# Kernel tuning notes

Measured on AMD Instinct MI355X. Metric: run time of the kernel, lower is better.

Reference implementation:

```python
import jax, jax.numpy as jnp
import numpy as np

N_NODES = 100000
N_EDGES = 3200000
D_FEAT = 128
N1 = 128
N2 = 64
NUM_CLASSES = 10
NUM_GRAPHS = 256


def gcn_conv(x, edge_index, W, b, num_nodes):
    """PyG GCNConv: y = D^-1/2 (A+I) D^-1/2 (x W) + b, self-loops added."""
    src, dst = edge_index[0], edge_index[1]
    # degree including self-loop (edge weight 1)
    deg = jax.ops.segment_sum(jnp.ones_like(dst, dtype=x.dtype), dst,
                              num_segments=num_nodes) + 1.0
    dis = jnp.where(deg > 0, deg ** -0.5, 0.0)  # deg_inv_sqrt, [N]
    h = x @ W                                    # transform first, [N, out]
    norm = dis[src] * dis[dst]                   # [E]
    msg = h[src] * norm[:, None]                 # gather + scale, [E, out]
    agg = jax.ops.segment_sum(msg, dst, num_segments=num_nodes)
    agg = agg + h * (dis * dis)[:, None]         # self-loop contribution
    return agg + b


def global_mean_pool(x, batch, num_graphs):
    sums = jax.ops.segment_sum(x, batch, num_segments=num_graphs)
    cnt = jax.ops.segment_sum(jnp.ones((x.shape[0],), dtype=x.dtype), batch,
                              num_segments=num_graphs)
    return sums / jnp.maximum(cnt, 1.0)[:, None]


def setup_inputs() -> dict:
    key = jax.random.key(0)
    ks = jax.random.split(key, 8)
    x = jax.random.normal(ks[0], (N_NODES, D_FEAT), dtype=jnp.float32)
    edge_index = jax.random.randint(ks[1], (2, N_EDGES), 0, N_NODES, dtype=jnp.int64)
    batch = jnp.sort(jax.random.randint(ks[2], (N_NODES,), 0, NUM_GRAPHS, dtype=jnp.int64))
    W1 = jax.random.normal(ks[3], (D_FEAT, N1), dtype=jnp.float32) / np.sqrt(D_FEAT)
    b1 = jnp.zeros((N1,), dtype=jnp.float32)
    W2 = jax.random.normal(ks[4], (N1, N2), dtype=jnp.float32) / np.sqrt(N1)
    b2 = jnp.zeros((N2,), dtype=jnp.float32)
    Wfc = jax.random.normal(ks[5], (N2, NUM_CLASSES), dtype=jnp.float32) / np.sqrt(N2)
    bfc = jnp.zeros((NUM_CLASSES,), dtype=jnp.float32)
    return {"x": x, "edge_index": edge_index, "batch": batch,
            "W1": W1, "b1": b1, "W2": W2, "b2": b2,
            "Wfc": Wfc, "bfc": bfc, "num_graphs": NUM_GRAPHS}


def reference(x, edge_index, batch, W1, b1, W2, b2, Wfc, bfc, num_graphs):
    n = x.shape[0]
    h = gcn_conv(x, edge_index, W1, b1, n)
    h = jax.nn.relu(h)
    h = gcn_conv(h, edge_index, W2, b2, n)
    g = global_mean_pool(h, batch, num_graphs)   # [num_graphs, N2]
    # dropout is identity at inference
    return g @ Wfc + bfc                          # [num_graphs, num_classes]
```

## Files before the change

kernel.cpp:

```cpp
#include <hip/hip_runtime.h>
#include <math.h>

typedef unsigned int  u32;
typedef unsigned short u16;

#define TILE1 8192
#define BKW   256
#define CAP   9216

typedef __attribute__((ext_vector_type(8))) short bf16x8;
typedef __attribute__((ext_vector_type(4))) float f32x4;
union frag_u { bf16x8 v; u32 u[4]; uint4 q; };

__device__ inline u32 bf16_rne(float f) {
    u32 u = __float_as_uint(f);
    return (u + 0x7FFFu + ((u >> 16) & 1u)) >> 16;
}
__device__ inline float bf_lo(u32 u) { return __uint_as_float(u << 16); }
__device__ inline float bf_hi(u32 u) { return __uint_as_float(u & 0xFFFF0000u); }

__device__ inline void add8(float* acc, uint4 q) {
    acc[0] += bf_lo(q.x); acc[1] += bf_hi(q.x);
    acc[2] += bf_lo(q.y); acc[3] += bf_hi(q.y);
    acc[4] += bf_lo(q.z); acc[5] += bf_hi(q.z);
    acc[6] += bf_lo(q.w); acc[7] += bf_hi(q.w);
}

__device__ inline u32 relu_pk(u32 v) {
    u32 s = v & 0x80008000u;
    u32 m = (s >> 15) * 0xFFFFu;
    return v & ~m;
}


__global__ __launch_bounds__(512) void k_part1(const int* __restrict__ ei,
                                               int* __restrict__ bucketCur,
                                               u32* __restrict__ tmp,
                                               int E, int N, int NBK) {
    __shared__ int hist[1024];
    __shared__ int base[512];
    const int tid = threadIdx.x;
    if (tid < NBK) { hist[tid] = 0; hist[512 + tid] = 0; }
    __syncthreads();

    const int rep = (tid & 1) << 9;
    const int t0 = blockIdx.x * TILE1;
    const int4* ei4s = (const int4*)ei;
    const int4* ei4d = (const int4*)(ei + E);
    const int q0 = t0 >> 2;
    const int QE = E >> 2;

    int sv[16], dv[16], key[16];
#pragma unroll
    for (int j = 0; j < 4; ++j) {
        int qi = q0 + j * 512 + tid;
        int4 s4 = make_int4(0, 0, 0, 0), d4 = make_int4(-1, -1, -1, -1);
        if (qi < QE) { s4 = ei4s[qi]; d4 = ei4d[qi]; }
        sv[4 * j + 0] = s4.x; dv[4 * j + 0] = d4.x;
        sv[4 * j + 1] = s4.y; dv[4 * j + 1] = d4.y;
        sv[4 * j + 2] = s4.z; dv[4 * j + 2] = d4.z;
        sv[4 * j + 3] = s4.w; dv[4 * j + 3] = d4.w;
    }
#pragma unroll
    for (int j = 0; j < 16; ++j) {
        key[j] = -1;
        if ((unsigned)dv[j] < (unsigned)N && (unsigned)sv[j] < (unsigned)N) {
            key[j] = dv[j] >> 8;
            atomicAdd(&hist[key[j] + rep], 1);
        }
    }
    __syncthreads();
    if (tid < NBK) {
        int tot = hist[tid] + hist[512 + tid];
        base[tid] = atomicAdd(&bucketCur[tid], tot);
        hist[tid] = 0;
    }
    __syncthreads();
#pragma unroll
    for (int j = 0; j < 16; ++j) {
        if (key[j] >= 0) {
            int slot = atomicAdd(&hist[key[j]], 1);
            int off = base[key[j]] + slot;
            if (off < CAP)
                tmp[(size_t)key[j] * CAP + off] =
                    ((u32)(dv[j] & 255) << 17) | (u32)sv[j];
        }
    }
}

__global__ __launch_bounds__(512) void k_part2(const int* __restrict__ bucketCnt,
                                               const u32* __restrict__ tmp,
                                               int* __restrict__ csr,
                                               int* __restrict__ rowptr,
                                               float* __restrict__ dis,
                                               int N, int NBK) {
    __shared__ int hist[256];
    __shared__ int ts[512];
    __shared__ int sStart;
    const int b = blockIdx.x;
    const int t = threadIdx.x;

    int myCnt = (t < NBK) ? bucketCnt[t] : 0;
    ts[t] = myCnt;
    __syncthreads();
    for (int off = 1; off < 512; off <<= 1) {
        int u = (t >= off) ? ts[t - off] : 0;
        __syncthreads();
        ts[t] += u;
        __syncthreads();
    }
    if (t == b) sStart = ts[t] - myCnt;
    if (b == 0 && t == NBK - 1) rowptr[N] = ts[t];
    __syncthreads();
    const int start = sStart;
    const int cnt = bucketCnt[b];
    const u32* src = tmp + (size_t)b * CAP;

    if (t < 256) hist[t] = 0;
    __syncthreads();
    for (int i = t; i < cnt; i += 512)
        atomicAdd(&hist[src[i] >> 17], 1);
    __syncthreads();

    int h = (t < 256) ? hist[t] : 0;
    ts[t] = h;
    __syncthreads();
    for (int off = 1; off < 512; off <<= 1) {
        int u = (t >= off) ? ts[t - off] : 0;
        __syncthreads();
        ts[t] += u;
        __syncthreads();
    }
    if (t < 256) hist[t] = ts[t] - h;
    __syncthreads();

    if (t < 256) {
        int gn = (b << 8) + t;
        if (gn < N) {
            int e0 = hist[t];
            int e1 = (t < 255) ? hist[t + 1] : cnt;
            rowptr[gn] = start + e0;
            dis[gn] = rsqrtf((float)(e1 - e0) + 1.0f);
        }
    }
    __syncthreads();

    for (int i = t; i < cnt; i += 512) {
        u32 v = src[i];
        int p = atomicAdd(&hist[v >> 17], 1);
        csr[start + p] = (int)(v & 0x1FFFFu);
    }
}


__global__ __launch_bounds__(256) void k_convW(
    const float* __restrict__ W1, const float* __restrict__ W2,
    u32* __restrict__ W1h, u32* __restrict__ W1l,
    u32* __restrict__ W2h, u32* __restrict__ W2l,
    int* __restrict__ bucketCur, int NBK)
{
    int idx = blockIdx.x * 256 + threadIdx.x;
    if (idx < NBK) bucketCur[idx] = 0;
    if (idx < 8192) {
        int n = idx >> 6, k = (idx & 63) * 2;
        float w0 = W1[k * 128 + n], w1 = W1[(k + 1) * 128 + n];
        u32 h0 = bf16_rne(w0), h1 = bf16_rne(w1);
        u32 l0 = bf16_rne(w0 - __uint_as_float(h0 << 16));
        u32 l1 = bf16_rne(w1 - __uint_as_float(h1 << 16));
        W1h[idx] = h0 | (h1 << 16);
        W1l[idx] = l0 | (l1 << 16);
    } else if (idx < 12288) {
        int i2 = idx - 8192;
        int n = i2 >> 6, k = (i2 & 63) * 2;
        float w0 = W2[k * 64 + n], w1 = W2[(k + 1) * 64 + n];
        u32 h0 = bf16_rne(w0), h1 = bf16_rne(w1);
        u32 l0 = bf16_rne(w0 - __uint_as_float(h0 << 16));
        u32 l1 = bf16_rne(w1 - __uint_as_float(h1 << 16));
        W2h[i2] = h0 | (h1 << 16);
        W2l[i2] = l0 | (l1 << 16);
    }
}


__global__ __launch_bounds__(256) void k_gemm1m(
    const float* __restrict__ X, const u32* __restrict__ Wh,
    const u32* __restrict__ Wl, const float* __restrict__ dis,
    u32* __restrict__ Hb, int M)
{
    __shared__ uint4 sW[2176];
    const int tid = threadIdx.x;
    const int ny = blockIdx.y;
    const uint4* Wh4 = (const uint4*)Wh;
    const uint4* Wl4 = (const uint4*)Wl;
#pragma unroll
    for (int i = 0; i < 4; ++i) {
        int idx = tid + i * 256;
        int l = idx >> 4, j = idx & 15;
        sW[l * 17 + j] = Wh4[(ny * 64 + l) * 16 + j];
        sW[1088 + l * 17 + j] = Wl4[(ny * 64 + l) * 16 + j];
    }
    __syncthreads();

    const int w = tid >> 6, lane = tid & 63;
    const int mrow = blockIdx.x * 64 + w * 16;
    const int m16 = lane & 15, quad = lane >> 4;
    int gm = mrow + m16; if (gm >= M) gm = M - 1;

    frag_u Ah[4], Al[4];
    const float* xr = X + (size_t)gm * 128;
#pragma unroll
    for (int kt = 0; kt < 4; ++kt) {
        int kb = kt * 32 + quad * 8;
        float4 xa = *(const float4*)(xr + kb);
        float4 xb = *(const float4*)(xr + kb + 4);
        float xe[8] = {xa.x, xa.y, xa.z, xa.w, xb.x, xb.y, xb.z, xb.w};
#pragma unroll
        for (int j = 0; j < 4; ++j) {
            u32 h0 = bf16_rne(xe[2 * j]),     h1 = bf16_rne(xe[2 * j + 1]);
            u32 l0 = bf16_rne(xe[2 * j]     - __uint_as_float(h0 << 16));
            u32 l1 = bf16_rne(xe[2 * j + 1] - __uint_as_float(h1 << 16));
            Ah[kt].u[j] = h0 | (h1 << 16);
            Al[kt].u[j] = l0 | (l1 << 16);
        }
    }

    float dv[4];
#pragma unroll
    for (int r = 0; r < 4; ++r) {
        int gR = mrow + quad * 4 + r;
        dv[r] = (gR < M) ? dis[gR] : 0.f;
    }

#pragma unroll
    for (int nt = 0; nt < 4; ++nt) {
        f32x4 acc = {0.f, 0.f, 0.f, 0.f};
        int l = nt * 16 + m16;
#pragma unroll
        for (int kt = 0; kt < 4; ++kt) {
            frag_u Bh, Bl;
            Bh.q = sW[l * 17 + kt * 4 + quad];
            Bl.q = sW[1088 + l * 17 + kt * 4 + quad];
            acc = __builtin_amdgcn_mfma_f32_16x16x32_bf16(Al[kt].v, Bh.v, acc, 0, 0, 0);
            acc = __builtin_amdgcn_mfma_f32_16x16x32_bf16(Ah[kt].v, Bl.v, acc, 0, 0, 0);
            acc = __builtin_amdgcn_mfma_f32_16x16x32_bf16(Ah[kt].v, Bh.v, acc, 0, 0, 0);
        }
#pragma unroll
        for (int r = 0; r < 4; ++r) {
            float vs = acc[r] * dv[r];
            float vo = __shfl_xor(vs, 1, 64);
            if ((m16 & 1) == 0) {
                int gR = mrow + quad * 4 + r;
                if (gR < M)
                    Hb[(size_t)gR * 64 + ny * 32 + nt * 8 + (m16 >> 1)] =
                        bf16_rne(vs) | (bf16_rne(vo) << 16);
            }
        }
    }
}


__global__ __launch_bounds__(256) void k_gemm2m(
    const u32* __restrict__ Xb, const u32* __restrict__ Wh,
    const u32* __restrict__ Wl, const float* __restrict__ dis,
    u32* __restrict__ Hb, int M)
{
    __shared__ uint4 sW[2176];
    const int tid = threadIdx.x;
    const uint4* Wh4 = (const uint4*)Wh;
    const uint4* Wl4 = (const uint4*)Wl;
#pragma unroll
    for (int i = 0; i < 4; ++i) {
        int idx = tid + i * 256;
        int l = idx >> 4, j = idx & 15;
        sW[l * 17 + j] = Wh4[l * 16 + j];
        sW[1088 + l * 17 + j] = Wl4[l * 16 + j];
    }
    __syncthreads();

    const int w = tid >> 6, lane = tid & 63;
    const int mrow = blockIdx.x * 64 + w * 16;
    const int m16 = lane & 15, quad = lane >> 4;
    int gm = mrow + m16; if (gm >= M) gm = M - 1;

    const uint4* X4 = (const uint4*)Xb;
    frag_u A[4];
#pragma unroll
    for (int kt = 0; kt < 4; ++kt) {
        A[kt].q = X4[(size_t)gm * 16 + kt * 4 + quad];
#pragma unroll
        for (int j = 0; j < 4; ++j) A[kt].u[j] = relu_pk(A[kt].u[j]);
    }

    float dv[4];
#pragma unroll
    for (int r = 0; r < 4; ++r) {
        int gR = mrow + quad * 4 + r;
        dv[r] = (gR < M) ? dis[gR] : 0.f;
    }

#pragma unroll
    for (int nt = 0; nt < 4; ++nt) {
        f32x4 acc = {0.f, 0.f, 0.f, 0.f};
        int l = nt * 16 + m16;
#pragma unroll
        for (int kt = 0; kt < 4; ++kt) {
            frag_u Bh, Bl;
            Bh.q = sW[l * 17 + kt * 4 + quad];
            Bl.q = sW[1088 + l * 17 + kt * 4 + quad];
            acc = __builtin_amdgcn_mfma_f32_16x16x32_bf16(A[kt].v, Bl.v, acc, 0, 0, 0);
            acc = __builtin_amdgcn_mfma_f32_16x16x32_bf16(A[kt].v, Bh.v, acc, 0, 0, 0);
        }
#pragma unroll
        for (int r = 0; r < 4; ++r) {
            float vs = acc[r] * dv[r];
            float vo = __shfl_xor(vs, 1, 64);
            if ((m16 & 1) == 0) {
                int gR = mrow + quad * 4 + r;
                if (gR < M)
                    Hb[(size_t)gR * 32 + nt * 8 + (m16 >> 1)] =
                        bf16_rne(vs) | (bf16_rne(vo) << 16);
            }
        }
    }
}


template <int PART>
__global__ __launch_bounds__(256) void k_agg1h(
    const int* __restrict__ rowptr, const int* __restrict__ csr,
    const float* __restrict__ dis, const uint4* __restrict__ Hb4,
    const float* __restrict__ bias, u32* __restrict__ AGGb, int N)
{
    int n = (blockIdx.x * 256 + threadIdx.x) >> 6;
    int lane = threadIdx.x & 63;
    int slot = lane >> 3;
    int li   = lane & 7;
    if (n >= N) return;
    int e = rowptr[n];
    const int s1 = rowptr[n + 1];
    const float dn = dis[n];
    const int q = PART * 8 + li;

    float acc[8];
#pragma unroll
    for (int j = 0; j < 8; ++j) acc[j] = 0.f;

    for (; e + 16 <= s1; e += 16) {
        int i0 = csr[e + slot];
        int i1 = csr[e + 8 + slot];
        uint4 q0 = Hb4[(size_t)i0 * 16 + q];
        uint4 q1 = Hb4[(size_t)i1 * 16 + q];
        add8(acc, q0); add8(acc, q1);
    }
    for (; e + 8 <= s1; e += 8) {
        int i0 = csr[e + slot];
        uint4 q0 = Hb4[(size_t)i0 * 16 + q];
        add8(acc, q0);
    }
    {
        int rem = s1 - e;
        int idx = -1;
        if (slot < rem) idx = csr[e + slot];
        else if (slot == rem) idx = n;
        if (idx >= 0) {
            uint4 qq = Hb4[(size_t)idx * 16 + q];
            add8(acc, qq);
        }
    }

#pragma unroll
    for (int j = 0; j < 8; ++j) {
        acc[j] += __shfl_xor(acc[j], 8, 64);
        acc[j] += __shfl_xor(acc[j], 16, 64);
        acc[j] += __shfl_xor(acc[j], 32, 64);
    }

    if (slot < 2) {
        float4 bv = ((const float4*)bias)[q * 2 + slot];
        float o0 = fmaf(dn, acc[4 * slot + 0], bv.x);
        float o1 = fmaf(dn, acc[4 * slot + 1], bv.y);
        float o2 = fmaf(dn, acc[4 * slot + 2], bv.z);
        float o3 = fmaf(dn, acc[4 * slot + 3], bv.w);
        uint2 p;
        p.x = bf16_rne(o0) | (bf16_rne(o1) << 16);
        p.y = bf16_rne(o2) | (bf16_rne(o3) << 16);
        ((uint2*)AGGb)[(size_t)n * 32 + q * 2 + slot] = p;
    }
}


__global__ __launch_bounds__(256) void k_agg2(
    const int* __restrict__ rowptr, const int* __restrict__ csr,
    const float* __restrict__ dis, const uint4* __restrict__ Hb4,
    const float* __restrict__ bias, u32* __restrict__ AGGb, int N)
{
    int n = (blockIdx.x * 256 + threadIdx.x) >> 6;
    int lane = threadIdx.x & 63;
    int slot = lane >> 3;
    int li   = lane & 7;
    if (n >= N) return;
    int e = rowptr[n];
    const int s1 = rowptr[n + 1];
    const float dn = dis[n];

    float acc[8];
#pragma unroll
    for (int j = 0; j < 8; ++j) acc[j] = 0.f;

    for (; e + 16 <= s1; e += 16) {
        int i0 = csr[e + slot];
        int i1 = csr[e + 8 + slot];
        uint4 q0 = Hb4[(size_t)i0 * 8 + li];
        uint4 q1 = Hb4[(size_t)i1 * 8 + li];
        add8(acc, q0); add8(acc, q1);
    }
    for (; e + 8 <= s1; e += 8) {
        int i0 = csr[e + slot];
        uint4 q0 = Hb4[(size_t)i0 * 8 + li];
        add8(acc, q0);
    }
    {
        int rem = s1 - e;
        int idx = -1;
        if (slot < rem) idx = csr[e + slot];
        else if (slot == rem) idx = n;
        if (idx >= 0) {
            uint4 q = Hb4[(size_t)idx * 8 + li];
            add8(acc, q);
        }
    }

#pragma unroll
    for (int j = 0; j < 8; ++j) {
        acc[j] += __shfl_xor(acc[j], 8, 64);
        acc[j] += __shfl_xor(acc[j], 16, 64);
        acc[j] += __shfl_xor(acc[j], 32, 64);
    }

    if (slot < 2) {
        float4 bv = ((const float4*)bias)[li * 2 + slot];
        float o0 = fmaf(dn, acc[4 * slot + 0], bv.x);
        float o1 = fmaf(dn, acc[4 * slot + 1], bv.y);
        float o2 = fmaf(dn, acc[4 * slot + 2], bv.z);
        float o3 = fmaf(dn, acc[4 * slot + 3], bv.w);
        uint2 p;
        p.x = bf16_rne(o0) | (bf16_rne(o1) << 16);
        p.y = bf16_rne(o2) | (bf16_rne(o3) << 16);
        ((uint2*)AGGb)[(size_t)n * 16 + li * 2 + slot] = p;
    }
}


__device__ inline int lower_bound(const int* __restrict__ b, int n, int v) {
    int lo = 0, hi = n;
    while (lo < hi) { int m = (lo + hi) >> 1; if (b[m] < v) lo = m + 1; else hi = m; }
    return lo;
}

__global__ __launch_bounds__(256) void k_poolfc(
    const int* __restrict__ batch, const u32* __restrict__ AGGb2,
    const float* __restrict__ Wfc, const float* __restrict__ bfc,
    float* __restrict__ out, int n)
{
    int g = blockIdx.x;
    int start = lower_bound(batch, n, g);
    int end   = lower_bound(batch, n, g + 1);
    int tid = threadIdx.x;
    int f = tid & 63, stripe = tid >> 6;
    int ui = f >> 1, hi = f & 1;
    float acc = 0.f;
    for (int i = start + stripe; i < end; i += 4) {
        u32 v = AGGb2[(size_t)i * 32 + ui];
        acc += hi ? bf_hi(v) : bf_lo(v);
    }
    __shared__ float red[256];
    __shared__ float mean[64];
    red[tid] = acc;
    __syncthreads();
    if (tid < 64) {
        float s = red[tid] + red[tid + 64] + red[tid + 128] + red[tid + 192];
        float c = (float)(end - start);
        mean[tid] = s / fmaxf(c, 1.0f);
    }
    __syncthreads();
    if (tid < 10) {
        float o = bfc[tid];
        for (int k = 0; k < 64; ++k)
            o = fmaf(mean[k], Wfc[k * 10 + tid], o);
        out[g * 10 + tid] = o;
    }
}


extern "C" void kernel_launch(void* const* d_in, const int* in_sizes, int n_in,
                              void* d_out, int out_size, void* d_ws, size_t ws_size,
                              hipStream_t stream)
{
    const float* x    = (const float*)d_in[0];
    const int*   ei   = (const int*)d_in[1];
    const int*   batch= (const int*)d_in[2];
    const float* W1   = (const float*)d_in[3];
    const float* b1   = (const float*)d_in[4];
    const float* W2   = (const float*)d_in[5];
    const float* b2   = (const float*)d_in[6];
    const float* Wfc  = (const float*)d_in[7];
    const float* bfc  = (const float*)d_in[8];
    float* out = (float*)d_out;

    const int N  = in_sizes[0] / 128;
    const int E  = in_sizes[1] / 2;
    const int ng = out_size / 10;

    const int NBK = (N + BKW - 1) / BKW;

    int*   rowptr    = (int*)d_ws;
    int*   bucketCur = rowptr + 102400;
    float* dis       = (float*)(bucketCur + 512);
    int*   csr       = (int*)(dis + 102400);
    u32*   tmp       = (u32*)(csr + E);
    u32*   Hb1       = tmp;
    u32*   agg2b     = tmp;
    u32*   agg1b     = (u32*)((int*)tmp + (size_t)N * 64);
    u16*   Hb2       = (u16*)((int*)agg1b + (size_t)N * 128);
    u32*   W1h       = (u32*)((int*)Hb2 + (size_t)N * 32);
    u32*   W1l       = W1h + 8192;
    u32*   W2h       = W1l + 8192;
    u32*   W2l       = W2h + 4096;

    k_convW<<<48, 256, 0, stream>>>(W1, W2, W1h, W1l, W2h, W2l, bucketCur, NBK);
    k_part1<<<(E + TILE1 - 1) / TILE1, 512, 0, stream>>>(ei, bucketCur, tmp, E, N, NBK);
    k_part2<<<NBK, 512, 0, stream>>>(bucketCur, tmp, csr, rowptr, dis, N, NBK);

    k_gemm1m<<<dim3((N + 63) / 64, 2), 256, 0, stream>>>(x, W1h, W1l, dis, Hb1, N);
    k_agg1h<0><<<(N + 3) / 4, 256, 0, stream>>>(rowptr, csr, dis, (const uint4*)Hb1, b1, agg1b, N);
    k_agg1h<1><<<(N + 3) / 4, 256, 0, stream>>>(rowptr, csr, dis, (const uint4*)Hb1, b1, agg1b, N);

    k_gemm2m<<<(N + 63) / 64, 256, 0, stream>>>(agg1b, W2h, W2l, dis, (u32*)Hb2, N);
    k_agg2<<<(N + 3) / 4, 256, 0, stream>>>(rowptr, csr, dis, (const uint4*)Hb2, b2, agg2b, N);

    k_poolfc<<<ng, 256, 0, stream>>>(batch, agg2b, Wfc, bfc, out, N);
}
```

Before: 398.8 us.

## Fuse weight bf16 split into GEMMs, merge agg1 halves, widen partition histogram

```diff
diff --git a/kernel.cpp b/kernel.cpp
--- a/kernel.cpp
+++ b/kernel.cpp
@@ -32,18 +32,26 @@
     return v & ~m;
 }
 
+__device__ inline void split_pk(float w0, float w1, u32& hp, u32& lp) {
+    u32 h0 = bf16_rne(w0), h1 = bf16_rne(w1);
+    u32 l0 = bf16_rne(w0 - __uint_as_float(h0 << 16));
+    u32 l1 = bf16_rne(w1 - __uint_as_float(h1 << 16));
+    hp = h0 | (h1 << 16);
+    lp = l0 | (l1 << 16);
+}
+
 
 __global__ __launch_bounds__(512) void k_part1(const int* __restrict__ ei,
                                                int* __restrict__ bucketCur,
                                                u32* __restrict__ tmp,
                                                int E, int N, int NBK) {
-    __shared__ int hist[1024];
-    __shared__ int base[512];
+    __shared__ int cnt[2048];
+    __shared__ int base[2048];
     const int tid = threadIdx.x;
-    if (tid < NBK) { hist[tid] = 0; hist[512 + tid] = 0; }
-    __syncthreads();
-
-    const int rep = (tid & 1) << 9;
+    for (int i = tid; i < 2048; i += 512) cnt[i] = 0;
+    __syncthreads();
+
+    const int rep = tid & 3;
     const int t0 = blockIdx.x * TILE1;
     const int4* ei4s = (const int4*)ei;
     const int4* ei4d = (const int4*)(ei + E);
@@ -66,21 +74,28 @@
         key[j] = -1;
         if ((unsigned)dv[j] < (unsigned)N && (unsigned)sv[j] < (unsigned)N) {
             key[j] = dv[j] >> 8;
-            atomicAdd(&hist[key[j] + rep], 1);
+            atomicAdd(&cnt[key[j] * 4 + rep], 1);
         }
     }
     __syncthreads();
     if (tid < NBK) {
-        int tot = hist[tid] + hist[512 + tid];
-        base[tid] = atomicAdd(&bucketCur[tid], tot);
-        hist[tid] = 0;
+        int c0 = cnt[tid * 4], c1 = cnt[tid * 4 + 1];
+        int c2 = cnt[tid * 4 + 2], c3 = cnt[tid * 4 + 3];
+        int b0 = atomicAdd(&bucketCur[tid], c0 + c1 + c2 + c3);
+        base[tid * 4 + 0] = b0;
+        base[tid * 4 + 1] = b0 + c0;
+        base[tid * 4 + 2] = b0 + c0 + c1;
+        base[tid * 4 + 3] = b0 + c0 + c1 + c2;
+        cnt[tid * 4 + 0] = 0; cnt[tid * 4 + 1] = 0;
+        cnt[tid * 4 + 2] = 0; cnt[tid * 4 + 3] = 0;
     }
     __syncthreads();
 #pragma unroll
     for (int j = 0; j < 16; ++j) {
         if (key[j] >= 0) {
-            int slot = atomicAdd(&hist[key[j]], 1);
-            int off = base[key[j]] + slot;
+            int idx = key[j] * 4 + rep;
+            int slot = atomicAdd(&cnt[idx], 1);
+            int off = base[idx] + slot;
             if (off < CAP)
                 tmp[(size_t)key[j] * CAP + off] =
                     ((u32)(dv[j] & 255) << 17) | (u32)sv[j];
@@ -153,51 +168,28 @@
 }
 
 
-__global__ __launch_bounds__(256) void k_convW(
-    const float* __restrict__ W1, const float* __restrict__ W2,
-    u32* __restrict__ W1h, u32* __restrict__ W1l,
-    u32* __restrict__ W2h, u32* __restrict__ W2l,
-    int* __restrict__ bucketCur, int NBK)
-{
-    int idx = blockIdx.x * 256 + threadIdx.x;
-    if (idx < NBK) bucketCur[idx] = 0;
-    if (idx < 8192) {
-        int n = idx >> 6, k = (idx & 63) * 2;
-        float w0 = W1[k * 128 + n], w1 = W1[(k + 1) * 128 + n];
-        u32 h0 = bf16_rne(w0), h1 = bf16_rne(w1);
-        u32 l0 = bf16_rne(w0 - __uint_as_float(h0 << 16));
-        u32 l1 = bf16_rne(w1 - __uint_as_float(h1 << 16));
-        W1h[idx] = h0 | (h1 << 16);
-        W1l[idx] = l0 | (l1 << 16);
-    } else if (idx < 12288) {
-        int i2 = idx - 8192;
-        int n = i2 >> 6, k = (i2 & 63) * 2;
-        float w0 = W2[k * 64 + n], w1 = W2[(k + 1) * 64 + n];
-        u32 h0 = bf16_rne(w0), h1 = bf16_rne(w1);
-        u32 l0 = bf16_rne(w0 - __uint_as_float(h0 << 16));
-        u32 l1 = bf16_rne(w1 - __uint_as_float(h1 << 16));
-        W2h[i2] = h0 | (h1 << 16);
-        W2l[i2] = l0 | (l1 << 16);
-    }
-}
-
-
 __global__ __launch_bounds__(256) void k_gemm1m(
-    const float* __restrict__ X, const u32* __restrict__ Wh,
-    const u32* __restrict__ Wl, const float* __restrict__ dis,
-    u32* __restrict__ Hb, int M)
+    const float* __restrict__ X, const float* __restrict__ W1,
+    const float* __restrict__ dis, u32* __restrict__ Hb, int M)
 {
     __shared__ uint4 sW[2176];
     const int tid = threadIdx.x;
     const int ny = blockIdx.y;
-    const uint4* Wh4 = (const uint4*)Wh;
-    const uint4* Wl4 = (const uint4*)Wl;
 #pragma unroll
     for (int i = 0; i < 4; ++i) {
         int idx = tid + i * 256;
         int l = idx >> 4, j = idx & 15;
-        sW[l * 17 + j] = Wh4[(ny * 64 + l) * 16 + j];
-        sW[1088 + l * 17 + j] = Wl4[(ny * 64 + l) * 16 + j];
+        int n = ny * 64 + l;
+        uint4 hq, lq;
+        u32* hp = (u32*)&hq; u32* lp = (u32*)&lq;
+#pragma unroll
+        for (int c = 0; c < 4; ++c) {
+            int kk = j * 4 + c;
+            split_pk(W1[(2 * kk) * 128 + n], W1[(2 * kk + 1) * 128 + n],
+                     hp[c], lp[c]);
+        }
+        sW[l * 17 + j] = hq;
+        sW[1088 + l * 17 + j] = lq;
     }
     __syncthreads();
 
@@ -215,13 +207,8 @@
         float4 xb = *(const float4*)(xr + kb + 4);
         float xe[8] = {xa.x, xa.y, xa.z, xa.w, xb.x, xb.y, xb.z, xb.w};
 #pragma unroll
-        for (int j = 0; j < 4; ++j) {
-            u32 h0 = bf16_rne(xe[2 * j]),     h1 = bf16_rne(xe[2 * j + 1]);
-            u32 l0 = bf16_rne(xe[2 * j]     - __uint_as_float(h0 << 16));
-            u32 l1 = bf16_rne(xe[2 * j + 1] - __uint_as_float(h1 << 16));
-            Ah[kt].u[j] = h0 | (h1 << 16);
-            Al[kt].u[j] = l0 | (l1 << 16);
-        }
+        for (int j = 0; j < 4; ++j)
+            split_pk(xe[2 * j], xe[2 * j + 1], Ah[kt].u[j], Al[kt].u[j]);
     }
 
     float dv[4];
@@ -260,20 +247,25 @@
 
 
 __global__ __launch_bounds__(256) void k_gemm2m(
-    const u32* __restrict__ Xb, const u32* __restrict__ Wh,
-    const u32* __restrict__ Wl, const float* __restrict__ dis,
-    u32* __restrict__ Hb, int M)
+    const u32* __restrict__ Xb, const float* __restrict__ W2,
+    const float* __restrict__ dis, u32* __restrict__ Hb, int M)
 {
     __shared__ uint4 sW[2176];
     const int tid = threadIdx.x;
-    const uint4* Wh4 = (const uint4*)Wh;
-    const uint4* Wl4 = (const uint4*)Wl;
 #pragma unroll
     for (int i = 0; i < 4; ++i) {
         int idx = tid + i * 256;
         int l = idx >> 4, j = idx & 15;
-        sW[l * 17 + j] = Wh4[l * 16 + j];
-        sW[1088 + l * 17 + j] = Wl4[l * 16 + j];
+        uint4 hq, lq;
+        u32* hp = (u32*)&hq; u32* lp = (u32*)&lq;
+#pragma unroll
+        for (int c = 0; c < 4; ++c) {
+            int kk = j * 4 + c;
+            split_pk(W2[(2 * kk) * 64 + l], W2[(2 * kk + 1) * 64 + l],
+                     hp[c], lp[c]);
+        }
+        sW[l * 17 + j] = hq;
+        sW[1088 + l * 17 + j] = lq;
     }
     __syncthreads();
 
@@ -325,21 +317,19 @@
 }
 
 
-template <int PART>
-__global__ __launch_bounds__(256) void k_agg1h(
+__global__ __launch_bounds__(256) void k_agg1(
     const int* __restrict__ rowptr, const int* __restrict__ csr,
     const float* __restrict__ dis, const uint4* __restrict__ Hb4,
     const float* __restrict__ bias, u32* __restrict__ AGGb, int N)
 {
     int n = (blockIdx.x * 256 + threadIdx.x) >> 6;
     int lane = threadIdx.x & 63;
-    int slot = lane >> 3;
-    int li   = lane & 7;
+    int slot = lane >> 4;
+    int li   = lane & 15;
     if (n >= N) return;
     int e = rowptr[n];
     const int s1 = rowptr[n + 1];
     const float dn = dis[n];
-    const int q = PART * 8 + li;
 
     float acc[8];
 #pragma unroll
@@ -347,14 +337,18 @@
 
     for (; e + 16 <= s1; e += 16) {
         int i0 = csr[e + slot];
-        int i1 = csr[e + 8 + slot];
-        uint4 q0 = Hb4[(size_t)i0 * 16 + q];
-        uint4 q1 = Hb4[(size_t)i1 * 16 + q];
-        add8(acc, q0); add8(acc, q1);
-    }
-    for (; e + 8 <= s1; e += 8) {
+        int i1 = csr[e + 4 + slot];
+        int i2 = csr[e + 8 + slot];
+        int i3 = csr[e + 12 + slot];
+        uint4 q0 = Hb4[(size_t)i0 * 16 + li];
+        uint4 q1 = Hb4[(size_t)i1 * 16 + li];
+        uint4 q2 = Hb4[(size_t)i2 * 16 + li];
+        uint4 q3 = Hb4[(size_t)i3 * 16 + li];
+        add8(acc, q0); add8(acc, q1); add8(acc, q2); add8(acc, q3);
+    }
+    for (; e + 4 <= s1; e += 4) {
         int i0 = csr[e + slot];
-        uint4 q0 = Hb4[(size_t)i0 * 16 + q];
+        uint4 q0 = Hb4[(size_t)i0 * 16 + li];
         add8(acc, q0);
     }
     {
@@ -363,20 +357,19 @@
         if (slot < rem) idx = csr[e + slot];
         else if (slot == rem) idx = n;
         if (idx >= 0) {
-            uint4 qq = Hb4[(size_t)idx * 16 + q];
-            add8(acc, qq);
+            uint4 q = Hb4[(size_t)idx * 16 + li];
+            add8(acc, q);
         }
     }
 
 #pragma unroll
     for (int j = 0; j < 8; ++j) {
-        acc[j] += __shfl_xor(acc[j], 8, 64);
         acc[j] += __shfl_xor(acc[j], 16, 64);
         acc[j] += __shfl_xor(acc[j], 32, 64);
     }
 
     if (slot < 2) {
-        float4 bv = ((const float4*)bias)[q * 2 + slot];
+        float4 bv = ((const float4*)bias)[li * 2 + slot];
         float o0 = fmaf(dn, acc[4 * slot + 0], bv.x);
         float o1 = fmaf(dn, acc[4 * slot + 1], bv.y);
         float o2 = fmaf(dn, acc[4 * slot + 2], bv.z);
@@ -384,7 +377,7 @@
         uint2 p;
         p.x = bf16_rne(o0) | (bf16_rne(o1) << 16);
         p.y = bf16_rne(o2) | (bf16_rne(o3) << 16);
-        ((uint2*)AGGb)[(size_t)n * 32 + q * 2 + slot] = p;
+        ((uint2*)AGGb)[(size_t)n * 32 + li * 2 + slot] = p;
     }
 }
 
@@ -522,20 +515,15 @@
     u32*   agg2b     = tmp;
     u32*   agg1b     = (u32*)((int*)tmp + (size_t)N * 64);
     u16*   Hb2       = (u16*)((int*)agg1b + (size_t)N * 128);
-    u32*   W1h       = (u32*)((int*)Hb2 + (size_t)N * 32);
-    u32*   W1l       = W1h + 8192;
-    u32*   W2h       = W1l + 8192;
-    u32*   W2l       = W2h + 4096;
-
-    k_convW<<<48, 256, 0, stream>>>(W1, W2, W1h, W1l, W2h, W2l, bucketCur, NBK);
+
+    hipMemsetAsync(bucketCur, 0, NBK * sizeof(int), stream);
     k_part1<<<(E + TILE1 - 1) / TILE1, 512, 0, stream>>>(ei, bucketCur, tmp, E, N, NBK);
     k_part2<<<NBK, 512, 0, stream>>>(bucketCur, tmp, csr, rowptr, dis, N, NBK);
 
-    k_gemm1m<<<dim3((N + 63) / 64, 2), 256, 0, stream>>>(x, W1h, W1l, dis, Hb1, N);
-    k_agg1h<0><<<(N + 3) / 4, 256, 0, stream>>>(rowptr, csr, dis, (const uint4*)Hb1, b1, agg1b, N);
-    k_agg1h<1><<<(N + 3) / 4, 256, 0, stream>>>(rowptr, csr, dis, (const uint4*)Hb1, b1, agg1b, N);
-
-    k_gemm2m<<<(N + 63) / 64, 256, 0, stream>>>(agg1b, W2h, W2l, dis, (u32*)Hb2, N);
+    k_gemm1m<<<dim3((N + 63) / 64, 2), 256, 0, stream>>>(x, W1, dis, Hb1, N);
+    k_agg1<<<(N + 3) / 4, 256, 0, stream>>>(rowptr, csr, dis, (const uint4*)Hb1, b1, agg1b, N);
+
+    k_gemm2m<<<(N + 63) / 64, 256, 0, stream>>>(agg1b, W2, dis, (u32*)Hb2, N);
     k_agg2<<<(N + 3) / 4, 256, 0, stream>>>(rowptr, csr, dis, (const uint4*)Hb2, b2, agg2b, N);
 
     k_poolfc<<<ng, 256, 0, stream>>>(batch, agg2b, Wfc, bfc, out, N);
```

Result: slower. 450.9 us (+13.1%).
